# Optimization experiments

Measured on AMD Instinct MI355X. Metric: run time of the kernel, lower is better.

The kernel has to match this reference:

```python
import jax, jax.numpy as jnp
import numpy as np

B, L, WORD, H = 16, 32, 512, 1024
HALF = H // 2
TEMP = 1.0


def setup_inputs() -> dict:
    key = jax.random.key(0)
    ks = jax.random.split(key, 12)
    sd = 0.05
    f32 = jnp.float32
    # torch LSTMCell combined bias with forget-gate bias = 1 (gate order i,f,g,o)
    b_lstm = jnp.concatenate([jnp.zeros(HALF), jnp.ones(HALF), jnp.zeros(2 * HALF)]).astype(f32)
    return {
        "sentence_embedding": jax.random.normal(ks[0], (B, L, WORD), f32),
        "length": jax.random.randint(ks[1], (B,), L // 2, L + 1),
        "W_ih_f": jax.random.normal(ks[2], (4 * HALF, WORD), f32) * sd,
        "W_hh_f": jax.random.normal(ks[3], (4 * HALF, HALF), f32) * sd,
        "b_f": b_lstm,
        "W_ih_b": jax.random.normal(ks[4], (4 * HALF, WORD), f32) * sd,
        "W_hh_b": jax.random.normal(ks[5], (4 * HALF, HALF), f32) * sd,
        "b_b": b_lstm,
        "W_rank1": jax.random.normal(ks[6], (256, WORD + 1), f32) * sd,
        "W_rank2": jax.random.normal(ks[7], (1, 256), f32) * sd,
        "W_comp": jax.random.normal(ks[8], (5 * H, 3 * H), f32) * 0.02,
        "b_comp": jnp.zeros((5 * H,), f32),
    }


def _lstm(xs, W_ih, W_hh, b):
    # xs: (L, B, D) -> hs, cs: (B, L, HALF); torch LSTMCell gate order i,f,g,o
    n = xs.shape[1]
    hdim = W_hh.shape[1]

    def step(carry, xt):
        h, c = carry
        g = xt @ W_ih.T + h @ W_hh.T + b
        i, f, gg, o = jnp.split(g, 4, axis=1)
        c = jax.nn.sigmoid(f) * c + jax.nn.sigmoid(i) * jnp.tanh(gg)
        h = jax.nn.sigmoid(o) * jnp.tanh(c)
        return (h, c), (h, c)

    init = (jnp.zeros((n, hdim), xs.dtype), jnp.zeros((n, hdim), xs.dtype))
    _, (hs, cs) = jax.lax.scan(step, init, xs)
    return hs.transpose(1, 0, 2), cs.transpose(1, 0, 2)


def _rev_padded(x, lengths):
    # reverse the first lengths[b] timesteps of each sequence, keep padding in place
    t = np.arange(x.shape[1])
    idx = np.where(t[None, :] < lengths[:, None], lengths[:, None] - 1 - t[None, :], t[None, :])
    return jnp.take_along_axis(x, jnp.asarray(idx)[:, :, None], axis=1)


def _rank_score(seg, W1, W2):
    l = seg.shape[0]
    pos = (2.0 * jnp.arange(l, dtype=seg.dtype) / l - 1.0)[:, None]
    xy = jnp.concatenate([seg, pos], axis=1)
    return jax.nn.relu(xy @ W1.T) @ W2.T  # (l, 1)


def _compose(lst, rst, xst, Wc, bc):
    # Nary tree-LSTM composition over (left, right, current) states; None -> zeros
    hx, cx = xst
    zero = jnp.zeros_like(hx)
    hl, cl = lst if lst is not None else (zero, zero)
    hr, cr = rst if rst is not None else (zero, zero)
    g = jnp.concatenate([hl, hr, hx], axis=1) @ Wc.T + bc  # (1, 5H)
    i, fl, fr, u, o = jnp.split(g, 5, axis=1)
    c = jax.nn.sigmoid(fl) * cl + jax.nn.sigmoid(fr) * cr + jax.nn.sigmoid(i) * jnp.tanh(u)
    h = jax.nn.sigmoid(o) * jnp.tanh(c)
    return h, c


def _build(emb, hs, cs, start, end, W1, W2, Wc, bc, sent, splits, record):
    if end == start:
        return None
    if end == start + 1:
        return (hs[start:start + 1], cs[start:start + 1])
    logits_t = _rank_score(emb[start:end], W1, W2).T  # (1, l)
    y_soft = jax.nn.softmax(logits_t / TEMP, axis=1)
    if record:
        k = int(jnp.argmax(y_soft[0]))
        splits[(sent, start, end)] = k
    else:
        k = splits[(sent, start, end)]
    hard = jnp.zeros_like(y_soft).at[0, k].set(1.0)
    gate = jax.lax.stop_gradient(hard - y_soft) + y_soft  # straight-through estimator
    h = gate @ hs[start:end]
    c = gate @ cs[start:end]
    pos = start + k
    left = _build(emb, hs, cs, start, pos, W1, W2, Wc, bc, sent, splits, record)
    right = _build(emb, hs, cs, pos + 1, end, W1, W2, Wc, bc, sent, splits, record)
    return _compose(left, right, (h, c), Wc, bc)


def _forward(sentence_embedding, length, W_ih_f, W_hh_f, b_f, W_ih_b, W_hh_b, b_b,
             W_rank1, W_rank2, W_comp, b_comp, splits, record):
    lengths = np.asarray(length)
    hs_f, cs_f = _lstm(sentence_embedding.transpose(1, 0, 2), W_ih_f, W_hh_f, b_f)
    x_bw = _rev_padded(sentence_embedding, lengths)
    hs_b, cs_b = _lstm(x_bw.transpose(1, 0, 2), W_ih_b, W_hh_b, b_b)
    hs_b = _rev_padded(hs_b, lengths)
    cs_b = _rev_padded(cs_b, lengths)
    hs = jnp.concatenate([hs_f, hs_b], axis=2)  # (B, L, H)
    cs = jnp.concatenate([cs_f, cs_b], axis=2)
    h_out, c_out = [], []
    for i in range(sentence_embedding.shape[0]):
        st = _build(sentence_embedding[i], hs[i], cs[i], 0, int(lengths[i]),
                    W_rank1, W_rank2, W_comp, b_comp, i, splits, record)
        h_out.append(st[0])
        c_out.append(st[1])
    return jnp.concatenate(h_out, axis=0), jnp.concatenate(c_out, axis=0)


def reference(sentence_embedding, length, W_ih_f, W_hh_f, b_f, W_ih_b, W_hh_b, b_b,
              W_rank1, W_rank2, W_comp, b_comp):
    return _forward(sentence_embedding, length, W_ih_f, W_hh_f, b_f,
                    W_ih_b, W_hh_b, b_b, W_rank1, W_rank2, W_comp, b_comp, {}, True)
```

## Files before the change

kernel.cpp:

```cpp
#include <hip/hip_runtime.h>
#include <math.h>

#define NB 16
#define SL 32
#define H5 5120
#define K3 3072

typedef __attribute__((ext_vector_type(8))) short short8;
typedef __attribute__((ext_vector_type(4))) float floatx4;
typedef __attribute__((ext_vector_type(4))) int intx4;

__device__ __forceinline__ float sigf(float x) { return 1.0f / (1.0f + expf(-x)); }

__device__ __forceinline__ unsigned short f2bf(float x) {
  union { float f; unsigned int u; } v;
  v.f = x;
  unsigned int r = v.u + 0x7FFFu + ((v.u >> 16) & 1u);
  return (unsigned short)(r >> 16);
}

__device__ __forceinline__ void bar32(int* flags, int idx, int mygen) {
  asm volatile("s_waitcnt vmcnt(0)" ::: "memory");
  __syncthreads();
  const int tid = threadIdx.x;
  if (tid == 0)
    __hip_atomic_store(&flags[idx], mygen, __ATOMIC_RELAXED,
                       __HIP_MEMORY_SCOPE_AGENT);
  if (tid < 64) {
    const int off = (tid & 7) * 4;
    int ok;
    do {
      intx4 f;
      asm volatile("global_load_dwordx4 %0, %1, off sc0 sc1\n\t"
                   "s_waitcnt vmcnt(0)"
                   : "=&v"(f) : "v"(flags + off) : "memory");
      ok = (f.x >= mygen) & (f.y >= mygen) & (f.z >= mygen) & (f.w >= mygen);
    } while (__all(ok) == 0);
  }
  __syncthreads();
}

__device__ __forceinline__ void bar_rounds(int* flags, int* gen, int bid, int mygen) {
  asm volatile("s_waitcnt vmcnt(0)" ::: "memory");
  __syncthreads();
  const int tid = threadIdx.x;
  if (tid < 64) {
    if (tid == 0)
      __hip_atomic_store(&flags[bid], mygen, __ATOMIC_RELAXED,
                         __HIP_MEMORY_SCOPE_AGENT);
    if (bid == 0) {
      int ok;
      do {
        intx4 f0, f1;
        asm volatile("global_load_dwordx4 %0, %2, off sc0 sc1\n\t"
                     "global_load_dwordx4 %1, %3, off sc0 sc1\n\t"
                     "s_waitcnt vmcnt(0)"
                     : "=&v"(f0), "=&v"(f1)
                     : "v"(flags + tid * 8), "v"(flags + tid * 8 + 4)
                     : "memory");
        ok = (f0.x >= mygen) & (f0.y >= mygen) & (f0.z >= mygen) & (f0.w >= mygen)
           & (f1.x >= mygen) & (f1.y >= mygen) & (f1.z >= mygen) & (f1.w >= mygen);
      } while (__all(ok) == 0);
      if (tid == 0)
        __hip_atomic_store(gen, mygen, __ATOMIC_RELAXED,
                           __HIP_MEMORY_SCOPE_AGENT);
    } else if (tid == 0) {
      while (__hip_atomic_load(gen, __ATOMIC_RELAXED,
                               __HIP_MEMORY_SCOPE_AGENT) < mygen)
        __builtin_amdgcn_s_sleep(2);
    }
  }
  __syncthreads();
}


__global__ void k_zero3(float* a, int na, float* b, int nb_, float* c, int nc) {
  const int stride = gridDim.x * blockDim.x;
  int i = blockIdx.x * blockDim.x + threadIdx.x;
  for (int k = i; k < na; k += stride) a[k] = 0.0f;
  for (int k = i; k < nb_; k += stride) b[k] = 0.0f;
  for (int k = i; k < nc; k += stride) c[k] = 0.0f;
}

__global__ void k_conv6(const float* s0, unsigned short* d0, int n0,
                        const float* s1, unsigned short* d1, int n1,
                        const float* s2, unsigned short* d2, int n2,
                        const float* s3, unsigned short* d3, int n3,
                        const float* s4, unsigned short* d4, int n4,
                        const float* s5, unsigned short* d5, int n5)
{
  const float* s; unsigned short* d; int n;
  switch (blockIdx.y) {
    case 0: s = s0; d = d0; n = n0; break;
    case 1: s = s1; d = d1; n = n1; break;
    case 2: s = s2; d = d2; n = n2; break;
    case 3: s = s3; d = d3; n = n3; break;
    case 4: s = s4; d = d4; n = n4; break;
    default: s = s5; d = d5; n = n5; break;
  }
  const int nf4 = n >> 2;
  for (int i = blockIdx.x * blockDim.x + threadIdx.x; i < nf4; i += gridDim.x * blockDim.x) {
    const float4 v = *(const float4*)&s[i * 4];
    ushort4 o;
    o.x = f2bf(v.x); o.y = f2bf(v.y); o.z = f2bf(v.z); o.w = f2bf(v.w);
    *(ushort4*)&d[i * 4] = o;
  }
}

__device__ void gemm_body(const float* __restrict__ A, const float* __restrict__ W,
                          float* __restrict__ out, int bx, int by)
{
  __shared__ __align__(16) float sm[2 * 16 * 68];
  float* As = sm;
  float* Ws = sm + 16 * 68;
  const int tid = threadIdx.x;
  const int tx = tid & 15, ty = tid >> 4;
  const int g0 = bx * 64, r0 = by * 64;
  float acc[4][4];
#pragma unroll
  for (int i = 0; i < 4; ++i)
#pragma unroll
    for (int j = 0; j < 4; ++j) acc[i][j] = 0.0f;
  const int ks = tid & 15, rr = tid >> 4;
  for (int kt = 0; kt < 512; kt += 16) {
#pragma unroll
    for (int rep = 0; rep < 4; ++rep) {
      As[ks * 68 + rep * 16 + rr] = A[(size_t)(r0 + rep * 16 + rr) * 512 + kt + ks];
      Ws[ks * 68 + rep * 16 + rr] = W[(size_t)(g0 + rep * 16 + rr) * 513 + kt + ks];
    }
    __syncthreads();
#pragma unroll
    for (int k = 0; k < 16; ++k) {
      const float4 a4 = *(const float4*)&As[k * 68 + ty * 4];
      const float4 w4 = *(const float4*)&Ws[k * 68 + tx * 4];
      const float av[4] = {a4.x, a4.y, a4.z, a4.w};
      const float wv[4] = {w4.x, w4.y, w4.z, w4.w};
#pragma unroll
      for (int i = 0; i < 4; ++i)
#pragma unroll
        for (int j = 0; j < 4; ++j) acc[i][j] += av[i] * wv[j];
    }
    __syncthreads();
  }
#pragma unroll
  for (int i = 0; i < 4; ++i) {
    const int r = r0 + ty * 4 + i;
    float4 o;
    o.x = acc[i][0]; o.y = acc[i][1]; o.z = acc[i][2]; o.w = acc[i][3];
    *(float4*)&out[(size_t)r * 256 + g0 + tx * 4] = o;
  }
}

__device__ void xproj_body(const unsigned short* __restrict__ embB,
                           const unsigned short* __restrict__ B,
                           float* __restrict__ out, int bx, int by)
{
  __shared__ __align__(16) unsigned short As[128 * 40];
  __shared__ __align__(16) unsigned short Bs[128 * 40];
  const int tid = threadIdx.x;
  const int g0 = bx * 128;
  const int r0 = by * 128;
  const int wave = tid >> 6, lane = tid & 63;
  const int wm = wave >> 1, wn = wave & 1;
  const int l15 = lane & 15, quad = lane >> 4;
  floatx4 acc[4][4];
#pragma unroll
  for (int mt = 0; mt < 4; ++mt)
#pragma unroll
    for (int nt = 0; nt < 4; ++nt) acc[mt][nt] = (floatx4){0.f, 0.f, 0.f, 0.f};
  for (int kt = 0; kt < 512; kt += 32) {
    __syncthreads();
#pragma unroll
    for (int p = 0; p < 2; ++p) {
      const int i = tid + p * 256;
      const int row = i >> 2, q = i & 3;
      *(uint4*)&As[row * 40 + q * 8] = *(const uint4*)&embB[(size_t)(r0 + row) * 512 + kt + q * 8];
      *(uint4*)&Bs[row * 40 + q * 8] = *(const uint4*)&B[(size_t)(g0 + row) * 512 + kt + q * 8];
    }
    __syncthreads();
    short8 af[4], bfr[4];
#pragma unroll
    for (int mt = 0; mt < 4; ++mt)
      af[mt] = *(const short8*)&As[(wm * 64 + mt * 16 + l15) * 40 + quad * 8];
#pragma unroll
    for (int nt = 0; nt < 4; ++nt)
      bfr[nt] = *(const short8*)&Bs[(wn * 64 + nt * 16 + l15) * 40 + quad * 8];
#pragma unroll
    for (int mt = 0; mt < 4; ++mt)
#pragma unroll
      for (int nt = 0; nt < 4; ++nt)
        acc[mt][nt] = __builtin_amdgcn_mfma_f32_16x16x32_bf16(af[mt], bfr[nt], acc[mt][nt], 0, 0, 0);
  }
#pragma unroll
  for (int nt = 0; nt < 4; ++nt) {
    const int col = g0 + wn * 64 + nt * 16 + l15;
#pragma unroll
    for (int mt = 0; mt < 4; ++mt)
#pragma unroll
      for (int i = 0; i < 4; ++i) {
        const int row = r0 + wm * 64 + mt * 16 + quad * 4 + i;
        out[(size_t)row * 2048 + col] = acc[mt][nt][i];
      }
  }
}

__global__ __launch_bounds__(256)
void k_proj(const float* __restrict__ emb, const float* __restrict__ Wr1,
            float* __restrict__ E1,
            const unsigned short* __restrict__ embB,
            const unsigned short* __restrict__ WfB,
            const unsigned short* __restrict__ WbB,
            float* __restrict__ Xf, float* __restrict__ Xb)
{
  const int bid = blockIdx.x;
  if (bid < 32) {
    gemm_body(emb, Wr1, E1, bid & 3, bid >> 2);
  } else {
    const int idx = bid - 32;
    const int bz = idx >> 6, rem = idx & 63;
    xproj_body(embB, bz ? WbB : WfB, bz ? Xb : Xf, rem & 15, rem >> 4);
  }
}

__global__ __launch_bounds__(256)
void k_mfma_gemm(const unsigned short* __restrict__ U, const unsigned short* __restrict__ WcB,
                 const float* __restrict__ bc, float* __restrict__ gB)
{
  __shared__ __align__(16) unsigned short As[128 * 40];
  __shared__ __align__(16) unsigned short Bs[64 * 40];
  const int bid = blockIdx.x;
  const int r0 = (bid / 80) * 128;
  const int g0 = (bid % 80) * 64;
  const int tid = threadIdx.x;
  const int wave = tid >> 6, lane = tid & 63;
  const int wm = wave >> 1, wn = wave & 1;
  const int l15 = lane & 15, quad = lane >> 4;
  floatx4 acc[4][2];
#pragma unroll
  for (int mf = 0; mf < 4; ++mf)
#pragma unroll
    for (int nt = 0; nt < 2; ++nt) acc[mf][nt] = (floatx4){0.f, 0.f, 0.f, 0.f};
  const int a_row = tid >> 2, a_q = tid & 3;
  for (int kt = 0; kt < K3; kt += 32) {
    __syncthreads();
#pragma unroll
    for (int p = 0; p < 2; ++p) {
      const int i = tid + p * 256;
      const int row = i >> 2, q = i & 3;
      *(uint4*)&As[row * 40 + q * 8] = *(const uint4*)&U[(size_t)(r0 + row) * K3 + kt + q * 8];
    }
    *(uint4*)&Bs[a_row * 40 + a_q * 8] = *(const uint4*)&WcB[(size_t)(g0 + a_row) * K3 + kt + a_q * 8];
    __syncthreads();
    short8 af[4], bfr[2];
#pragma unroll
    for (int mf = 0; mf < 4; ++mf)
      af[mf] = *(const short8*)&As[(wm * 64 + mf * 16 + l15) * 40 + quad * 8];
#pragma unroll
    for (int nt = 0; nt < 2; ++nt)
      bfr[nt] = *(const short8*)&Bs[(wn * 32 + nt * 16 + l15) * 40 + quad * 8];
#pragma unroll
    for (int mf = 0; mf < 4; ++mf)
#pragma unroll
      for (int nt = 0; nt < 2; ++nt)
        acc[mf][nt] = __builtin_amdgcn_mfma_f32_16x16x32_bf16(af[mf], bfr[nt], acc[mf][nt], 0, 0, 0);
  }
#pragma unroll
  for (int nt = 0; nt < 2; ++nt) {
    const int col = g0 + wn * 32 + nt * 16 + l15;
    const float bias = bc[col];
#pragma unroll
    for (int mf = 0; mf < 4; ++mf)
#pragma unroll
      for (int i = 0; i < 4; ++i) {
        const int row = r0 + wm * 64 + mf * 16 + quad * 4 + i;
        gB[(size_t)row * H5 + col] = acc[mf][nt][i] + bias;
      }
  }
}

__device__ void scan_body(const float* __restrict__ Xf, const float* __restrict__ Xb,
                          const unsigned short* __restrict__ WhfB,
                          const unsigned short* __restrict__ WhbB,
                          const float* __restrict__ bf, const float* __restrict__ bb,
                          const int* __restrict__ len,
                          unsigned short* __restrict__ hbB, float* __restrict__ cbuf,
                          float* __restrict__ hs, float* __restrict__ cs,
                          int* __restrict__ bar, int bid)
{
  const int dir = bid >> 5;
  const int hjt = bid & 31;
  const int tid = threadIdx.x;
  const int wave = tid >> 6, lane = tid & 63;
  const int l15 = lane & 15, quad = lane >> 4;
  const unsigned short* Wh = dir ? WhbB : WhfB;
  const float* bias = dir ? bb : bf;
  const float* X = dir ? Xb : Xf;
  int* myflags = &bar[528 + dir * 32];
  __shared__ float sg[4 * 16 * 17];
  const int jg = wave * 512 + hjt * 16 + l15;
  short8 wfr[16];
#pragma unroll
  for (int k8 = 0; k8 < 16; ++k8)
    wfr[k8] = *(const short8*)&Wh[(size_t)jg * 512 + k8 * 32 + quad * 8];
  const int bb_ = tid >> 4, j = tid & 15;
  const int hj = hjt * 16 + j;
  const int Lb = len[bb_];
  const float bi_i = bias[hj];
  const float bi_f = bias[512 + hj];
  const float bi_g = bias[1024 + hj];
  const float bi_o = bias[1536 + hj];
  for (int t = 0; t < SL; ++t) {
    const int pp = t & 1;
    const unsigned short* hp = hbB + (size_t)(dir * 2 + pp) * 8192;
    unsigned short* hn = hbB + (size_t)(dir * 2 + (pp ^ 1)) * 8192;
    const float* cp = cbuf + (size_t)(dir * 2 + pp) * 8192;
    float* cn = cbuf + (size_t)(dir * 2 + (pp ^ 1)) * 8192;
    int xidx = t;
    if (dir) xidx = (t < Lb) ? (Lb - 1 - t) : t;
    const float* xr = X + (size_t)(bb_ * SL + xidx) * 2048;
    const float x0 = xr[hj];
    const float x1 = xr[512 + hj];
    const float x2 = xr[1024 + hj];
    const float x3 = xr[1536 + hj];
    const float cprev = cp[bb_ * 512 + hj];
    short8 afr[16];
#pragma unroll
    for (int k8 = 0; k8 < 16; ++k8)
      asm volatile("global_load_dwordx4 %0, %1, off sc0 sc1"
                   : "=&v"(afr[k8])
                   : "v"(&hp[(size_t)l15 * 512 + k8 * 32 + quad * 8]));
    asm volatile("s_waitcnt vmcnt(0)" ::: "memory");
    __builtin_amdgcn_sched_barrier(0);
    floatx4 acc = (floatx4){0.f, 0.f, 0.f, 0.f};
#pragma unroll
    for (int k8 = 0; k8 < 16; ++k8)
      acc = __builtin_amdgcn_mfma_f32_16x16x32_bf16(afr[k8], wfr[k8], acc, 0, 0, 0);
#pragma unroll
    for (int i = 0; i < 4; ++i)
      sg[wave * 272 + (quad * 4 + i) * 17 + l15] = acc[i];
    __syncthreads();
    const float gi = sg[0 * 272 + bb_ * 17 + j] + x0 + bi_i;
    const float gf = sg[1 * 272 + bb_ * 17 + j] + x1 + bi_f;
    const float gg = sg[2 * 272 + bb_ * 17 + j] + x2 + bi_g;
    const float go = sg[3 * 272 + bb_ * 17 + j] + x3 + bi_o;
    const float cnew = sigf(gf) * cprev + sigf(gi) * tanhf(gg);
    const float hnew = sigf(go) * tanhf(cnew);
    cn[bb_ * 512 + hj] = cnew;
    const unsigned int hb16 = f2bf(hnew);
    asm volatile("global_store_short %0, %1, off sc0 sc1"
                 :: "v"(&hn[bb_ * 512 + hj]), "v"(hb16) : "memory");
    const int pos = dir ? xidx : t;
    const int col = dir ? (512 + hj) : hj;
    hs[(size_t)(bb_ * SL + pos) * 1024 + col] = hnew;
    cs[(size_t)(bb_ * SL + pos) * 1024 + col] = cnew;
    if (t != SL - 1) bar32(myflags, hjt, t + 1);
  }
}

__device__ void score_body(const float* __restrict__ E1, const float* __restrict__ Wr1,
                           const float* __restrict__ Wr2, const int* __restrict__ len,
                           int* __restrict__ ksplit, int b, int s)
{
  const int L = len[b];
  if (s + 2 > L) return;
  const int tid = threadIdx.x;
  __shared__ float e[32 * 257];
  __shared__ float w1p[256];
  __shared__ float w2s[256];
  __shared__ float red[32 * 8];
  __shared__ float sc[32];
  const int nrow = 32 - s;
  for (int i = tid; i < nrow * 256; i += 256) {
    const int rr = i >> 8, q = i & 255;
    e[rr * 257 + q] = E1[(size_t)(b * SL + s + rr) * 256 + q];
  }
  w1p[tid] = Wr1[tid * 513 + 512];
  w2s[tid] = Wr2[tid];
  __syncthreads();
  const int t_ = tid & 31, jg = tid >> 5;
  const int lmax = L - s;
  for (int l = 2; l <= lmax; ++l) {
    float part = 0.0f;
    if (t_ < l) {
      const float pos = 2.0f * (float)t_ / (float)l - 1.0f;
      const float* er = e + t_ * 257;
      for (int q = jg * 32; q < jg * 32 + 32; ++q) {
        const float v = er[q] + pos * w1p[q];
        part += fmaxf(v, 0.0f) * w2s[q];
      }
    }
    red[t_ * 8 + jg] = part;
    __syncthreads();
    if (jg == 0 && t_ < l) {
      float su = 0.0f;
      for (int q = 0; q < 8; ++q) su += red[t_ * 8 + q];
      sc[t_] = su;
    }
    __syncthreads();
    if (tid == 0) {
      int k = 0;
      float best = sc[0];
      for (int q = 1; q < l; ++q)
        if (sc[q] > best) { best = sc[q]; k = q; }
      ksplit[(b * 32 + s) * 33 + l] = k;
    }
    __syncthreads();
  }
}

__global__ __launch_bounds__(256)
void k_scansc(const float* Xf, const float* Xb,
              const unsigned short* WhfB, const unsigned short* WhbB,
              const float* bf, const float* bb, const int* len,
              unsigned short* hbB, float* cbuf, float* hs, float* cs, int* bar,
              const float* E1, const float* Wr1, const float* Wr2, int* ksplit)
{
  const int bid = blockIdx.x;
  if (bid < 64) {
    scan_body(Xf, Xb, WhfB, WhbB, bf, bb, len, hbB, cbuf, hs, cs, bar, bid);
  } else {
    const int idx = bid - 64;
    score_body(E1, Wr1, Wr2, len, ksplit, idx / 31, idx % 31);
  }
}

__global__ __launch_bounds__(64)
void k_walk(const int* __restrict__ ksplit, const int* __restrict__ len,
            int* __restrict__ meta)
{
  const int b = blockIdx.x;
  const int tid = threadIdx.x;
  __shared__ int ks[32 * 33];
  __shared__ int stk[96];
  for (int i = tid; i < 32 * 33; i += 64) ks[i] = ksplit[b * 1056 + i];
  __syncthreads();
  if (tid != 0) return;
  int* own = meta;
  int* lt = meta + 512;
  int* li = meta + 1024;
  int* rt = meta + 1536;
  int* ri = meta + 2048;
  int* dep = meta + 2560;
  int* nn = meta + 3072;
  int* dcnt = meta + 3088;
  int* lcnt = meta + 3120;
  int* dlist = meta + 3152;
  int* llist = meta + 19536;
  int sp = 0, nn_ = 1;
  stk[0] = 0; stk[1] = len[b]; stk[2] = 0;
  sp = 1;
  while (sp > 0) {
    sp--;
    const int s = stk[sp * 3], eN = stk[sp * 3 + 1], nid = stk[sp * 3 + 2];
    const int l = eN - s;
    const int k = ks[s * 33 + l];
    const int m = b * 32 + nid;
    own[m] = s + k;
    if (k == 0) { lt[m] = 0; li[m] = 0; }
    else if (k == 1) { lt[m] = 1; li[m] = s; }
    else {
      const int id = nn_++;
      lt[m] = 2; li[m] = id;
      stk[sp * 3] = s; stk[sp * 3 + 1] = s + k; stk[sp * 3 + 2] = id; sp++;
    }
    const int rl = l - k - 1;
    if (rl == 0) { rt[m] = 0; ri[m] = 0; }
    else if (rl == 1) { rt[m] = 1; ri[m] = s + k + 1; }
    else {
      const int id = nn_++;
      rt[m] = 2; ri[m] = id;
      stk[sp * 3] = s + k + 1; stk[sp * 3 + 1] = eN; stk[sp * 3 + 2] = id; sp++;
    }
  }
  nn[b] = nn_;
  for (int i = nn_ - 1; i >= 0; --i) {
    const int m = b * 32 + i;
    int d = 1;
    if (lt[m] == 2) d = max(d, dep[b * 32 + li[m]] + 1);
    if (rt[m] == 2) d = max(d, dep[b * 32 + ri[m]] + 1);
    dep[m] = d;
  }
  for (int i = 0; i < nn_; ++i) {
    const int m = b * 32 + i;
    const int r = dep[m];
    const int idx = atomicAdd(&dcnt[r], 1);
    dlist[r * 512 + idx] = m;
    if (lt[m] == 2 || rt[m] == 2) {
      const int lx = atomicAdd(&lcnt[r], 1);
      llist[r * 512 + lx] = m;
    }
  }
}

__global__ __launch_bounds__(256)
void k_ubuild(const float* __restrict__ hs, const int* __restrict__ meta,
              unsigned short* __restrict__ U)
{
  const int id = blockIdx.x, b = blockIdx.y;
  const int tid = threadIdx.x;
  const int* own = meta;
  const int* lt = meta + 512;
  const int* li = meta + 1024;
  const int* rt = meta + 1536;
  const int* ri = meta + 2048;
  const int* nn = meta + 3072;
  const int m = b * 32 + id;
  unsigned short* u = U + (size_t)m * K3;
  if (id >= nn[b]) {
    for (int i = tid; i < K3; i += 256) u[i] = 0;
    return;
  }
  const float* hl = (lt[m] == 1) ? hs + (size_t)(b * 32 + li[m]) * 1024 : nullptr;
  const float* hr = (rt[m] == 1) ? hs + (size_t)(b * 32 + ri[m]) * 1024 : nullptr;
  const float* hx = hs + (size_t)(b * 32 + own[m]) * 1024;
  for (int i = tid; i < 1024; i += 256) {
    u[i] = hl ? f2bf(hl[i]) : 0;
    u[1024 + i] = hr ? f2bf(hr[i]) : 0;
    u[2048 + i] = f2bf(hx[i]);
  }
}

__global__ __launch_bounds__(256, 2)
void k_rounds(const unsigned short* __restrict__ WcB, const int* __restrict__ meta,
              unsigned short* __restrict__ nodehb,
              const float* __restrict__ gB, const float* __restrict__ cs,
              float* __restrict__ nodec,
              float* __restrict__ out, int* __restrict__ bar,
              const unsigned short* __restrict__ zpad)
{
  const int* lt = meta + 512;
  const int* li = meta + 1024;
  const int* rt = meta + 1536;
  const int* ri = meta + 2048;
  const int* dcnt = meta + 3088;
  const int* dlist = meta + 3152;
  __shared__ float scratch[4][16][17];
  __shared__ float gates[16][17];
  const int tid = threadIdx.x;
  const int bid = blockIdx.x;
  const int wave = tid >> 6, lane = tid & 63;
  const int l15 = lane & 15, quad = lane >> 4;
  const int j0 = bid * 2;
  const int cc = (l15 < 10) ? l15 : l15 - 10;
  const size_t wrow = (size_t)((cc >> 1) * 1024 + j0 + (cc & 1)) * K3;
  const int kbase = wave * 256 + quad * 8;
  short8 wreg[16];
#pragma unroll
  for (int i = 0; i < 8; ++i) {
    wreg[i]     = *(const short8*)&WcB[wrow + kbase + i * 32];
    wreg[8 + i] = *(const short8*)&WcB[wrow + 1024 + kbase + i * 32];
  }
  const int rnd = tid >> 4, rc = tid & 15;
  int bgen = 0;
  for (int r = 1; r <= 31; ++r) {
    const int cnt = dcnt[r];
    if (cnt == 0) break;
    if (r >= 2) { ++bgen; bar_rounds(bar, &bar[512], bid, bgen); }
    for (int c0 = 0; c0 < cnt; c0 += 16) {
      float gBv = 0.0f;
      if (rc < 10 && c0 + rnd < cnt) {
        const int nodeP = dlist[r * 512 + c0 + rnd];
        gBv = gB[(size_t)nodeP * H5 + (rc >> 1) * 1024 + j0 + (rc & 1)];
      }
      const int ma = c0 + l15;
      const unsigned short* pl = zpad;
      const unsigned short* pr = zpad;
      if (ma < cnt) {
        const int node = dlist[r * 512 + ma];
        const int base = node & ~31;
        if (lt[node] == 2) pl = nodehb + (size_t)(base + li[node]) * 1024;
        if (rt[node] == 2) pr = nodehb + (size_t)(base + ri[node]) * 1024;
      }
      short8 al[8], ar[8];
#pragma unroll
      for (int i = 0; i < 8; ++i)
        asm volatile("global_load_dwordx4 %0, %1, off sc0 sc1"
                     : "=&v"(al[i]) : "v"(pl + kbase + i * 32));
#pragma unroll
      for (int i = 0; i < 8; ++i)
        asm volatile("global_load_dwordx4 %0, %1, off sc0 sc1"
                     : "=&v"(ar[i]) : "v"(pr + kbase + i * 32));
      floatx4 acc = (floatx4){0.f, 0.f, 0.f, 0.f};
      asm volatile("s_waitcnt vmcnt(8)" ::: "memory");
      __builtin_amdgcn_sched_barrier(0);
#pragma unroll
      for (int ks = 0; ks < 8; ++ks)
        acc = __builtin_amdgcn_mfma_f32_16x16x32_bf16(al[ks], wreg[ks], acc, 0, 0, 0);
      asm volatile("s_waitcnt vmcnt(0)" ::: "memory");
      __builtin_amdgcn_sched_barrier(0);
#pragma unroll
      for (int ks = 0; ks < 8; ++ks)
        acc = __builtin_amdgcn_mfma_f32_16x16x32_bf16(ar[ks], wreg[8 + ks], acc, 0, 0, 0);
      __syncthreads();
#pragma unroll
      for (int i = 0; i < 4; ++i)
        scratch[wave][quad * 4 + i][l15] = acc[i];
      __syncthreads();
      if (rc < 10)
        gates[rnd][rc] = gBv + scratch[0][rnd][rc] + scratch[1][rnd][rc]
                             + scratch[2][rnd][rc] + scratch[3][rnd][rc];
      __syncthreads();
      if (tid < 16) {
        const int mc = c0 + tid;
        if (mc < cnt) {
          const int node = dlist[r * 512 + mc];
          const int base = node & ~31;
          const int ltv = lt[node], rtv = rt[node];
          const float* clp = (ltv == 2) ? &nodec[(size_t)(base + li[node]) * 1024]
                           : (ltv == 1) ? &cs[(size_t)(base + li[node]) * 1024] : nullptr;
          const float* crp = (rtv == 2) ? &nodec[(size_t)(base + ri[node]) * 1024]
                           : (rtv == 1) ? &cs[(size_t)(base + ri[node]) * 1024] : nullptr;
          unsigned int pk = 0;
#pragma unroll
          for (int jj = 0; jj < 2; ++jj) {
            const int j = j0 + jj;
            const float gi  = gates[tid][0 + jj];
            const float gfl = gates[tid][2 + jj];
            const float gfr = gates[tid][4 + jj];
            const float gu  = gates[tid][6 + jj];
            const float go  = gates[tid][8 + jj];
            const float cl = clp ? clp[j] : 0.0f;
            const float cr = crp ? crp[j] : 0.0f;
            const float c_ = sigf(gfl) * cl + sigf(gfr) * cr + sigf(gi) * tanhf(gu);
            const float h  = sigf(go) * tanhf(c_);
            nodec[(size_t)node * 1024 + j] = c_;
            pk |= ((unsigned int)f2bf(h)) << (16 * jj);
            if ((node & 31) == 0) {
              const int b = node >> 5;
              out[b * 1024 + j] = h;
              out[16384 + b * 1024 + j] = c_;
            }
          }
          asm volatile("global_store_dword %0, %1, off sc0 sc1"
                       :: "v"(nodehb + (size_t)node * 1024 + j0), "v"(pk)
                       : "memory");
        }
      }
    }
  }
}

extern "C" void kernel_launch(void* const* d_in, const int* in_sizes, int n_in,
                              void* d_out, int out_size, void* d_ws, size_t ws_size,
                              hipStream_t stream) {
  const float* emb = (const float*)d_in[0];
  const int* len = (const int*)d_in[1];
  const float* Wihf = (const float*)d_in[2];
  const float* Whhf = (const float*)d_in[3];
  const float* bf = (const float*)d_in[4];
  const float* Wihb = (const float*)d_in[5];
  const float* Whhb = (const float*)d_in[6];
  const float* bb = (const float*)d_in[7];
  const float* Wr1 = (const float*)d_in[8];
  const float* Wr2 = (const float*)d_in[9];
  const float* Wc = (const float*)d_in[10];
  const float* bc = (const float*)d_in[11];
  float* out = (float*)d_out;

  float* ws = (float*)d_ws;
  float* Xf = ws;
  float* Xb = Xf + 1048576;
  float* hs = Xb + 1048576;
  float* cs = hs + 524288;
  float* E1 = cs + 524288;
  unsigned short* U = (unsigned short*)(E1 + 131072);
  float* gB = (float*)U + 786432;
  float* nodeh = gB + 2621440;
  float* nodec = nodeh + 524288;
  unsigned short* nodehb = (unsigned short*)(nodec + 524288);
  float* cbuf = (float*)nodehb + 262144;
  unsigned short* hbB = (unsigned short*)(cbuf + 32768);
  unsigned short* WcB = (unsigned short*)((float*)hbB + 16384);
  unsigned short* WihfB = WcB + 15728640;
  unsigned short* WihbB = WihfB + 1048576;
  unsigned short* WhhfB = WihbB + 1048576;
  unsigned short* WhhbB = WhhfB + 1048576;
  unsigned short* embB = WhhbB + 1048576;
  int* meta = (int*)(embB + 262144);
  int* ksplit = meta + 36096;
  int* bar = ksplit + 16896;
  unsigned short* zpad = (unsigned short*)(bar + 1024);

  k_zero3<<<128, 256, 0, stream>>>(cbuf, 49152, (float*)(meta + 3088), 64,
                                   (float*)bar, 1536);
  k_conv6<<<dim3(1920, 6), 256, 0, stream>>>(
      Wc, WcB, 15728640, Wihf, WihfB, 1048576, Wihb, WihbB, 1048576,
      Whhf, WhhfB, 1048576, Whhb, WhhbB, 1048576, emb, embB, 262144);
  k_proj<<<160, 256, 0, stream>>>(emb, Wr1, E1, embB, WihfB, WihbB, Xf, Xb);
  k_scansc<<<560, 256, 0, stream>>>(Xf, Xb, WhhfB, WhhbB, bf, bb, len, hbB,
                                    cbuf, hs, cs, bar, E1, Wr1, Wr2, ksplit);
  k_walk<<<16, 64, 0, stream>>>(ksplit, len, meta);
  k_ubuild<<<dim3(32, 16), 256, 0, stream>>>(hs, meta, U);
  k_mfma_gemm<<<320, 256, 0, stream>>>(U, WcB, bc, gB);
  k_rounds<<<512, 256, 0, stream>>>(WcB, meta, nodehb, gB, cs,
                                    nodec, out, bar, zpad);
}
```

Measured before the change: 550.1 us.

## Overlap W_comp bf16 conversion and tree walk with the LSTM scan kernel

Moves the large W_comp fp32-to-bf16 conversion out of the up-front conversion kernel and into extra blocks of the scan/score kernel, so it runs alongside the latency-bound sequential LSTM scan. The split-tree walk also becomes extra blocks in that kernel, spin-waiting on per-(batch,start) completion flags that the score blocks publish with agent-scope atomics, which removes a separate launch. The gain depends on these blocks being co-resident with the scan. The risks are spin-wait deadlock if the walk blocks occupy slots the score blocks need, and bandwidth contention with the scan.

Result: faster. 510.1 us (-7.3%).

```diff
diff --git a/kernel.cpp b/kernel.cpp
--- a/kernel.cpp
+++ b/kernel.cpp
@@ -82,12 +82,11 @@
   for (int k = i; k < nc; k += stride) c[k] = 0.0f;
 }
 
-__global__ void k_conv6(const float* s0, unsigned short* d0, int n0,
+__global__ void k_conv5(const float* s0, unsigned short* d0, int n0,
                         const float* s1, unsigned short* d1, int n1,
                         const float* s2, unsigned short* d2, int n2,
                         const float* s3, unsigned short* d3, int n3,
-                        const float* s4, unsigned short* d4, int n4,
-                        const float* s5, unsigned short* d5, int n5)
+                        const float* s4, unsigned short* d4, int n4)
 {
   const float* s; unsigned short* d; int n;
   switch (blockIdx.y) {
@@ -95,8 +94,7 @@
     case 1: s = s1; d = d1; n = n1; break;
     case 2: s = s2; d = d2; n = n2; break;
     case 3: s = s3; d = d3; n = n3; break;
-    case 4: s = s4; d = d4; n = n4; break;
-    default: s = s5; d = d5; n = n5; break;
+    default: s = s4; d = d4; n = n4; break;
   }
   const int nf4 = n >> 2;
   for (int i = blockIdx.x * blockDim.x + threadIdx.x; i < nf4; i += gridDim.x * blockDim.x) {
@@ -359,80 +357,84 @@
 
 __device__ void score_body(const float* __restrict__ E1, const float* __restrict__ Wr1,
                            const float* __restrict__ Wr2, const int* __restrict__ len,
-                           int* __restrict__ ksplit, int b, int s)
-{
+                           int* __restrict__ ksplit, int* __restrict__ sflag,
+                           int b, int s)
+{
+  const int tid = threadIdx.x;
   const int L = len[b];
-  if (s + 2 > L) return;
-  const int tid = threadIdx.x;
-  __shared__ float e[32 * 257];
-  __shared__ float w1p[256];
-  __shared__ float w2s[256];
-  __shared__ float red[32 * 8];
-  __shared__ float sc[32];
-  const int nrow = 32 - s;
-  for (int i = tid; i < nrow * 256; i += 256) {
-    const int rr = i >> 8, q = i & 255;
-    e[rr * 257 + q] = E1[(size_t)(b * SL + s + rr) * 256 + q];
-  }
-  w1p[tid] = Wr1[tid * 513 + 512];
-  w2s[tid] = Wr2[tid];
+  if (s + 2 <= L) {
+    __shared__ float e[32 * 257];
+    __shared__ float w1p[256];
+    __shared__ float w2s[256];
+    __shared__ float red[32 * 8];
+    __shared__ float sc[32];
+    const int nrow = 32 - s;
+    for (int i = tid; i < nrow * 256; i += 256) {
+      const int rr = i >> 8, q = i & 255;
+      e[rr * 257 + q] = E1[(size_t)(b * SL + s + rr) * 256 + q];
+    }
+    w1p[tid] = Wr1[tid * 513 + 512];
+    w2s[tid] = Wr2[tid];
+    __syncthreads();
+    const int t_ = tid & 31, jg = tid >> 5;
+    const int lmax = L - s;
+    for (int l = 2; l <= lmax; ++l) {
+      float part = 0.0f;
+      if (t_ < l) {
+        const float pos = 2.0f * (float)t_ / (float)l - 1.0f;
+        const float* er = e + t_ * 257;
+        for (int q = jg * 32; q < jg * 32 + 32; ++q) {
+          const float v = er[q] + pos * w1p[q];
+          part += fmaxf(v, 0.0f) * w2s[q];
+        }
+      }
+      red[t_ * 8 + jg] = part;
+      __syncthreads();
+      if (jg == 0 && t_ < l) {
+        float su = 0.0f;
+        for (int q = 0; q < 8; ++q) su += red[t_ * 8 + q];
+        sc[t_] = su;
+      }
+      __syncthreads();
+      if (tid == 0) {
+        int k = 0;
+        float best = sc[0];
+        for (int q = 1; q < l; ++q)
+          if (sc[q] > best) { best = sc[q]; k = q; }
+        __hip_atomic_store(&ksplit[(b * 32 + s) * 33 + l], k,
+                           __ATOMIC_RELAXED, __HIP_MEMORY_SCOPE_AGENT);
+      }
+      __syncthreads();
+    }
+  }
   __syncthreads();
-  const int t_ = tid & 31, jg = tid >> 5;
-  const int lmax = L - s;
-  for (int l = 2; l <= lmax; ++l) {
-    float part = 0.0f;
-    if (t_ < l) {
-      const float pos = 2.0f * (float)t_ / (float)l - 1.0f;
-      const float* er = e + t_ * 257;
-      for (int q = jg * 32; q < jg * 32 + 32; ++q) {
-        const float v = er[q] + pos * w1p[q];
-        part += fmaxf(v, 0.0f) * w2s[q];
-      }
-    }
-    red[t_ * 8 + jg] = part;
-    __syncthreads();
-    if (jg == 0 && t_ < l) {
-      float su = 0.0f;
-      for (int q = 0; q < 8; ++q) su += red[t_ * 8 + q];
-      sc[t_] = su;
-    }
-    __syncthreads();
-    if (tid == 0) {
-      int k = 0;
-      float best = sc[0];
-      for (int q = 1; q < l; ++q)
-        if (sc[q] > best) { best = sc[q]; k = q; }
-      ksplit[(b * 32 + s) * 33 + l] = k;
-    }
-    __syncthreads();
-  }
-}
-
-__global__ __launch_bounds__(256)
-void k_scansc(const float* Xf, const float* Xb,
-              const unsigned short* WhfB, const unsigned short* WhbB,
-              const float* bf, const float* bb, const int* len,
-              unsigned short* hbB, float* cbuf, float* hs, float* cs, int* bar,
-              const float* E1, const float* Wr1, const float* Wr2, int* ksplit)
-{
-  const int bid = blockIdx.x;
-  if (bid < 64) {
-    scan_body(Xf, Xb, WhfB, WhbB, bf, bb, len, hbB, cbuf, hs, cs, bar, bid);
-  } else {
-    const int idx = bid - 64;
-    score_body(E1, Wr1, Wr2, len, ksplit, idx / 31, idx % 31);
-  }
-}
-
-__global__ __launch_bounds__(64)
-void k_walk(const int* __restrict__ ksplit, const int* __restrict__ len,
-            int* __restrict__ meta)
-{
-  const int b = blockIdx.x;
-  const int tid = threadIdx.x;
+  if (tid == 0) {
+    asm volatile("s_waitcnt vmcnt(0)" ::: "memory");
+    __hip_atomic_store(&sflag[b * 31 + s], 1,
+                       __ATOMIC_RELAXED, __HIP_MEMORY_SCOPE_AGENT);
+  }
+}
+
+__device__ void walk_body(const int* __restrict__ ksplit, const int* __restrict__ len,
+                          int* __restrict__ meta, int* __restrict__ sflag, int b)
+{
+  const int tid = threadIdx.x;
+  if (tid < 64) {
+    int ok;
+    do {
+      int v = 1;
+      if (tid < 31)
+        v = __hip_atomic_load(&sflag[b * 31 + tid], __ATOMIC_RELAXED,
+                              __HIP_MEMORY_SCOPE_AGENT);
+      ok = (v != 0);
+    } while (__all(ok) == 0);
+  }
+  __syncthreads();
   __shared__ int ks[32 * 33];
   __shared__ int stk[96];
-  for (int i = tid; i < 32 * 33; i += 64) ks[i] = ksplit[b * 1056 + i];
+  for (int i = tid; i < 32 * 33; i += 256)
+    ks[i] = __hip_atomic_load(&ksplit[b * 1056 + i], __ATOMIC_RELAXED,
+                              __HIP_MEMORY_SCOPE_AGENT);
   __syncthreads();
   if (tid != 0) return;
   int* own = meta;
@@ -493,6 +495,34 @@
 }
 
 __global__ __launch_bounds__(256)
+void k_scansc(const float* Xf, const float* Xb,
+              const unsigned short* WhfB, const unsigned short* WhbB,
+              const float* bf, const float* bb, const int* len,
+              unsigned short* hbB, float* cbuf, float* hs, float* cs, int* bar,
+              const float* E1, const float* Wr1, const float* Wr2, int* ksplit,
+              const float* Wc, unsigned short* WcB, int* sflag, int* meta)
+{
+  const int bid = blockIdx.x;
+  if (bid < 64) {
+    scan_body(Xf, Xb, WhfB, WhbB, bf, bb, len, hbB, cbuf, hs, cs, bar, bid);
+  } else if (bid < 560) {
+    const int idx = bid - 64;
+    score_body(E1, Wr1, Wr2, len, ksplit, sflag, idx / 31, idx % 31);
+  } else if (bid < 688) {
+    const int idx = bid - 560;
+    const int nf4 = 15728640 >> 2;
+    for (int i = idx * 256 + threadIdx.x; i < nf4; i += 128 * 256) {
+      const float4 v = *(const float4*)&Wc[i * 4];
+      ushort4 o;
+      o.x = f2bf(v.x); o.y = f2bf(v.y); o.z = f2bf(v.z); o.w = f2bf(v.w);
+      *(ushort4*)&WcB[i * 4] = o;
+    }
+  } else {
+    walk_body(ksplit, len, meta, sflag, bid - 688);
+  }
+}
+
+__global__ __launch_bounds__(256)
 void k_ubuild(const float* __restrict__ hs, const int* __restrict__ meta,
               unsigned short* __restrict__ U)
 {
@@ -680,16 +710,17 @@
   int* ksplit = meta + 36096;
   int* bar = ksplit + 16896;
   unsigned short* zpad = (unsigned short*)(bar + 1024);
+  int* sflag = bar + 1536;
 
   k_zero3<<<128, 256, 0, stream>>>(cbuf, 49152, (float*)(meta + 3088), 64,
-                                   (float*)bar, 1536);
-  k_conv6<<<dim3(1920, 6), 256, 0, stream>>>(
-      Wc, WcB, 15728640, Wihf, WihfB, 1048576, Wihb, WihbB, 1048576,
-      Whhf, WhhfB, 1048576, Whhb, WhhbB, 1048576, emb, embB, 262144);
+                                   (float*)bar, 2048);
+  k_conv5<<<dim3(512, 5), 256, 0, stream>>>(
+      emb, embB, 262144, Wihf, WihfB, 1048576, Wihb, WihbB, 1048576,
+      Whhf, WhhfB, 1048576, Whhb, WhhbB, 1048576);
   k_proj<<<160, 256, 0, stream>>>(emb, Wr1, E1, embB, WihfB, WihbB, Xf, Xb);
-  k_scansc<<<560, 256, 0, stream>>>(Xf, Xb, WhhfB, WhhbB, bf, bb, len, hbB,
-                                    cbuf, hs, cs, bar, E1, Wr1, Wr2, ksplit);
-  k_walk<<<16, 64, 0, stream>>>(ksplit, len, meta);
+  k_scansc<<<704, 256, 0, stream>>>(Xf, Xb, WhhfB, WhhbB, bf, bb, len, hbB,
+                                    cbuf, hs, cs, bar, E1, Wr1, Wr2, ksplit,
+                                    Wc, WcB, sflag, meta);
   k_ubuild<<<dim3(32, 16), 256, 0, stream>>>(hs, meta, U);
   k_mfma_gemm<<<320, 256, 0, stream>>>(U, WcB, bc, gB);
   k_rounds<<<512, 256, 0, stream>>>(WcB, meta, nodehb, gB, cs,
```
